# Kernel tuning notes

Hardware: AMD Instinct MI355X
Metric: run time of the kernel (lower is better)

## Reference

```python
import jax, jax.numpy as jnp
import numpy as np

CONF_THRESHOLD = 4.0
NMS_THRESHOLD = 0.5
TOP_K = 4096        # fixed candidate cap for jit-static shapes (>> expected #candidates)
NEG = -1.0e9


def setup_inputs() -> dict:
    key = jax.random.key(0)
    k1, k2, k3 = jax.random.split(key, 3)
    B, N, C = 8, 65536, 80
    logits = jax.random.normal(k1, (B, N, C), dtype=jnp.float32)
    # valid xyxy boxes in a ~1000px image: x2>x1, y2>y1
    xy = jax.random.uniform(k2, (B, N, 2), dtype=jnp.float32) * 900.0
    wh = jax.random.uniform(k3, (B, N, 2), dtype=jnp.float32) * 100.0 + 1.0
    boxes = jnp.concatenate([xy, xy + wh], axis=-1)
    return {"logits": logits, "boxes": boxes}


def _pairwise_iou(b):
    # b: [K, 4] xyxy -> [K, K] IoU (torchvision convention, no +1)
    x1, y1, x2, y2 = b[:, 0], b[:, 1], b[:, 2], b[:, 3]
    area = (x2 - x1) * (y2 - y1)                      # [K]
    iw = jnp.maximum(jnp.minimum(x2[:, None], x2[None, :]) - jnp.maximum(x1[:, None], x1[None, :]), 0.0)
    ih = jnp.maximum(jnp.minimum(y2[:, None], y2[None, :]) - jnp.maximum(y1[:, None], y1[None, :]), 0.0)
    inter = iw * ih                                   # [K, K]
    union = area[:, None] + area[None, :] - inter
    return inter / jnp.maximum(union, 1e-12)


def reference(logits, boxes):
    B, N, C = logits.shape
    scores = jnp.max(logits, axis=2)                  # [B, N]
    cls = jnp.argmax(logits, axis=2)                  # [B, N]
    # per-(image, class) NMS category id, as in the torch module
    cat = cls + jnp.arange(B, dtype=cls.dtype)[:, None] * C
    valid = scores > CONF_THRESHOLD                   # [B, N]
    img = jnp.broadcast_to(jnp.arange(B, dtype=jnp.int32)[:, None], (B, N))

    scores_f = scores.reshape(-1)
    valid_f = valid.reshape(-1)
    boxes_f = boxes.reshape(-1, 4)
    cat_f = cat.reshape(-1)
    cls_f = cls.reshape(-1)
    img_f = img.reshape(-1)

    # global descending-score order (matches batched_nms sort); invalid pushed to bottom
    vals, idx = jax.lax.top_k(jnp.where(valid_f, scores_f, NEG), TOP_K)
    bx = boxes_f[idx]                                 # [K, 4]
    ct = cat_f[idx]
    cl = cls_f[idx]
    im = img_f[idx]
    vk = valid_f[idx]                                 # [K]

    iou = _pairwise_iou(bx)                           # [K, K]
    suppress_mat = (ct[:, None] == ct[None, :]) & (iou > NMS_THRESHOLD)
    order = jnp.arange(TOP_K)

    def body(i, keep):
        sup = suppress_mat[i] & (order > i)
        return jnp.where(keep[i], keep & ~sup, keep)

    keep = jax.lax.fori_loop(0, TOP_K, body, vk)      # greedy NMS suppression

    nms_image_idx = jnp.where(keep, im, -1)
    nms_bboxes = bx * keep[:, None].astype(bx.dtype)
    nms_classes = jnp.where(keep, cl, -1)
    nms_scores = jnp.where(keep, vals, 0.0)
    return (nms_image_idx, nms_bboxes, nms_classes, nms_scores)
```

## Files before the change

kernel.cpp:

```cpp
#include <hip/hip_runtime.h>
#include <stdint.h>

typedef unsigned long long u64;
typedef unsigned int u32;
typedef float fv4 __attribute__((ext_vector_type(4)));

#define BATCH  8
#define NPTS   65536
#define NCLS   80
#define NANCH  (BATCH * NPTS)
#define TOPK   4096
#define CONF   4.0f
#define NMSTH  0.5f
#define NCAT   (BATCH * NCLS)
#define BCAP   32

static constexpr size_t OFF_CNT  = 0;
static constexpr size_t OFF_KEYS = 64;

__global__ __launch_bounds__(256, 4) void k_score(const float* __restrict__ logits,
                                                  int* __restrict__ cnt,
                                                  u64* __restrict__ keys) {
    __shared__ u32 s_sc[4][64 * 21];
    __shared__ unsigned char s_cl[4][64 * 20];
    int lane = threadIdx.x & 63;
    int w = threadIdx.x >> 6;
    int chunk = blockIdx.x * 4 + w;
    const fv4* src = (const fv4*)logits + (size_t)chunk * 1280;

    fv4 A[20];
#pragma unroll
    for (int k = 0; k < 20; ++k) A[k] = __builtin_nontemporal_load(&src[k * 64 + lane]);

    u32* sc = s_sc[w];
    unsigned char* cl = s_cl[w];

#pragma unroll
    for (int k = 0; k < 20; ++k) {
        fv4 v = A[k];
        int e = k * 64 + lane;
        float bv = v.x; int bc = 0;
        if (v.y > bv) { bv = v.y; bc = 1; }
        if (v.z > bv) { bv = v.z; bc = 2; }
        if (v.w > bv) { bv = v.w; bc = 3; }
        int a_l = e / 20, j = e % 20;
        u32 eb = __float_as_uint(bv);
        eb = (eb & 0x80000000u) ? ~eb : (eb | 0x80000000u);
        sc[a_l * 21 + j] = eb;
        cl[a_l * 20 + j] = (unsigned char)(j * 4 + bc);
    }
    u32 best = 0; int bj = 0;
#pragma unroll
    for (int j = 0; j < 20; ++j) {
        u32 p = sc[lane * 21 + j];
        if (p > best) { best = p; bj = j; }
    }
    u32 orig = (best & 0x80000000u) ? (best & 0x7fffffffu) : ~best;
    if (__uint_as_float(orig) > CONF) {
        u32 cls = cl[lane * 20 + bj];
        u32 a = (u32)chunk * 64 + (u32)lane;
        int pos = atomicAdd(cnt, 1);
        if (pos < 8192)
            keys[pos] = ((u64)best << 32) | ((((~a) & 0x7FFFFu) << 7) | cls);
    }
}

__global__ __launch_bounds__(1024) void k_nms(const int* __restrict__ cnt,
                                              const u64* __restrict__ keys_raw,
                                              const float* __restrict__ boxes,
                                              float* __restrict__ out) {
    __shared__ u64    s_keys[4096];
    __shared__ float4 s_box[4096];
    __shared__ unsigned short s_bucket[NCAT * BCAP];
    __shared__ int s_bcnt[NCAT];
    __shared__ unsigned char s_keep[4096];
    int n = min(*cnt, TOPK);
    int tid = threadIdx.x;
    int n2 = 64; while (n2 < n) n2 <<= 1;

    for (int c = tid; c < NCAT; c += 1024) s_bcnt[c] = 0;
    for (int i = tid; i < n2; i += 1024)
        s_keys[i] = (i < n) ? keys_raw[i] : 0ull;
    __syncthreads();

    for (int k = 2; k <= n2; k <<= 1) {
        for (int j = k >> 1; j > 0; j >>= 1) {
            for (int i = tid; i < n2; i += 1024) {
                int ixj = i ^ j;
                if (ixj > i) {
                    u64 x = s_keys[i], y = s_keys[ixj];
                    bool desc = ((i & k) == 0);
                    if (desc ? (x < y) : (x > y)) { s_keys[i] = y; s_keys[ixj] = x; }
                }
            }
            __syncthreads();
        }
    }

    float4 bx[4]; int cls_[4], img_[4]; float sc_[4];
#pragma unroll
    for (int r = 0; r < 4; ++r) {
        int s = tid + 1024 * r;
        float4 b = make_float4(0.f, 0.f, 0.f, 0.f);
        int cl = -1, im = -1; float v = 0.f;
        if (s < n) {
            u64 key = s_keys[s];
            u32 eb = (u32)(key >> 32);
            u32 orig = (eb & 0x80000000u) ? (eb & 0x7fffffffu) : ~eb;
            v = __uint_as_float(orig);
            u32 low = (u32)key;
            cl = (int)(low & 0x7fu);
            u32 a = (~(low >> 7)) & 0x7FFFFu;
            im = (int)(a >> 16);
            b = ((const float4*)boxes)[a];
            int c = im * NCLS + cl;
            int pos = atomicAdd(&s_bcnt[c], 1);
            if (pos < BCAP) s_bucket[c * BCAP + pos] = (unsigned short)s;
        }
        bx[r] = b; cls_[r] = cl; img_[r] = im; sc_[r] = v;
        s_box[s]  = b;
        s_keep[s] = (s < n) ? 1 : 0;
    }
    __syncthreads();

    if (tid < NCAT) {
        int m = min(s_bcnt[tid], BCAP);
        unsigned short* bkt = &s_bucket[tid * BCAP];
        if (m > 1) {
            for (int i = 1; i < m; ++i) {
                unsigned short x = bkt[i]; int j = i - 1;
                while (j >= 0 && bkt[j] > x) { bkt[j + 1] = bkt[j]; --j; }
                bkt[j + 1] = x;
            }
            for (int i = 1; i < m; ++i) {
                float4 bi = s_box[bkt[i]];
                float areai = (bi.z - bi.x) * (bi.w - bi.y);
                bool dead = false;
                for (int j = 0; j < i && !dead; ++j) {
                    if (!s_keep[bkt[j]]) continue;
                    float4 bj = s_box[bkt[j]];
                    float iw = fmaxf(fminf(bi.z, bj.z) - fmaxf(bi.x, bj.x), 0.f);
                    float ih = fmaxf(fminf(bi.w, bj.w) - fmaxf(bi.y, bj.y), 0.f);
                    float inter = iw * ih;
                    float uni = areai + (bj.z - bj.x) * (bj.w - bj.y) - inter;
                    if (inter / fmaxf(uni, 1e-12f) > NMSTH) dead = true;
                }
                if (dead) s_keep[bkt[i]] = 0;
            }
        }
    }
    __syncthreads();

#pragma unroll
    for (int r = 0; r < 4; ++r) {
        int s = tid + 1024 * r;
        bool keep = s_keep[s] != 0;
        out[s] = keep ? (float)img_[r] : -1.0f;
        ((float4*)(out + 4096))[s] = keep ? bx[r] : make_float4(0.f, 0.f, 0.f, 0.f);
        out[4096 + 16384 + s]        = keep ? (float)cls_[r] : -1.0f;
        out[4096 + 16384 + 4096 + s] = keep ? sc_[r] : 0.0f;
    }
}

extern "C" void kernel_launch(void* const* d_in, const int* in_sizes, int n_in,
                              void* d_out, int out_size, void* d_ws, size_t ws_size,
                              hipStream_t stream) {
    const float* logits = (const float*)d_in[0];
    const float* boxes  = (const float*)d_in[1];
    float* out = (float*)d_out;
    char* ws = (char*)d_ws;

    int* cnt      = (int*)(ws + OFF_CNT);
    u64* keys_raw = (u64*)(ws + OFF_KEYS);

    hipMemsetAsync(cnt, 0, 64, stream);
    k_score<<<NANCH / 256, 256, 0, stream>>>(logits, cnt, keys_raw);
    k_nms<<<1, 1024, 0, stream>>>(cnt, keys_raw, boxes, out);
}
```

Before: 270.7 us.

## Replace global atomic candidate append with per-chunk ballot slots and NMS-side compaction

The scoring kernel no longer does a global atomicAdd per candidate. Each wavefront ballots its passing anchors and writes them into a fixed 16-entry slot per 64-anchor chunk, then stores a per-chunk count. This also removes the memset. The NMS kernel reads all 8192 chunk counts and compacts the slots into shared memory with a shared atomic. This trades global atomic contention for an extra scan of the count array in the single-block NMS kernel. Candidates beyond 16 per chunk would be dropped, which is safe for the expected sparsity.

```diff
diff --git a/kernel.cpp b/kernel.cpp
--- a/kernel.cpp
+++ b/kernel.cpp
@@ -9,18 +9,20 @@
 #define NPTS   65536
 #define NCLS   80
 #define NANCH  (BATCH * NPTS)
+#define NCHUNK (NANCH / 64)
 #define TOPK   4096
 #define CONF   4.0f
 #define NMSTH  0.5f
 #define NCAT   (BATCH * NCLS)
 #define BCAP   32
-
-static constexpr size_t OFF_CNT  = 0;
-static constexpr size_t OFF_KEYS = 64;
+#define SLOT   16
+
+static constexpr size_t OFF_CNTS = 0;
+static constexpr size_t OFF_SLAB = 32768;
 
 __global__ __launch_bounds__(256, 4) void k_score(const float* __restrict__ logits,
-                                                  int* __restrict__ cnt,
-                                                  u64* __restrict__ keys) {
+                                                  u32* __restrict__ cnts,
+                                                  u64* __restrict__ slab) {
     __shared__ u32 s_sc[4][64 * 21];
     __shared__ unsigned char s_cl[4][64 * 20];
     int lane = threadIdx.x & 63;
@@ -56,17 +58,26 @@
         if (p > best) { best = p; bj = j; }
     }
     u32 orig = (best & 0x80000000u) ? (best & 0x7fffffffu) : ~best;
-    if (__uint_as_float(orig) > CONF) {
-        u32 cls = cl[lane * 20 + bj];
-        u32 a = (u32)chunk * 64 + (u32)lane;
-        int pos = atomicAdd(cnt, 1);
-        if (pos < 8192)
-            keys[pos] = ((u64)best << 32) | ((((~a) & 0x7FFFFu) << 7) | cls);
+    bool pred = __uint_as_float(orig) > CONF;
+
+    u64 ball = __ballot(pred);
+    if (pred) {
+        int slot = __popcll(ball & ((1ull << lane) - 1ull));
+        if (slot < SLOT) {
+            u32 cls = cl[lane * 20 + bj];
+            u32 a = (u32)chunk * 64 + (u32)lane;
+            slab[(size_t)chunk * SLOT + slot] =
+                ((u64)best << 32) | ((((~a) & 0x7FFFFu) << 7) | cls);
+        }
+    }
+    if (lane == 0) {
+        int m = (int)__popcll(ball);
+        cnts[chunk] = (u32)(m < SLOT ? m : SLOT);
     }
 }
 
-__global__ __launch_bounds__(1024) void k_nms(const int* __restrict__ cnt,
-                                              const u64* __restrict__ keys_raw,
+__global__ __launch_bounds__(1024) void k_nms(const u32* __restrict__ cnts,
+                                              const u64* __restrict__ slab,
                                               const float* __restrict__ boxes,
                                               float* __restrict__ out) {
     __shared__ u64    s_keys[4096];
@@ -74,14 +85,28 @@
     __shared__ unsigned short s_bucket[NCAT * BCAP];
     __shared__ int s_bcnt[NCAT];
     __shared__ unsigned char s_keep[4096];
-    int n = min(*cnt, TOPK);
+    __shared__ int s_n;
     int tid = threadIdx.x;
+
+    if (tid == 0) s_n = 0;
+    for (int c = tid; c < NCAT; c += 1024) s_bcnt[c] = 0;
+    for (int i = tid; i < 4096; i += 1024) s_keys[i] = 0ull;
+    __syncthreads();
+
+    for (int c = tid; c < NCHUNK; c += 1024) {
+        int m = (int)cnts[c];
+        if (m > 0) {
+            int pos = atomicAdd(&s_n, m);
+            for (int t = 0; t < m; ++t) {
+                int p = pos + t;
+                if (p < TOPK) s_keys[p] = slab[(size_t)c * SLOT + t];
+            }
+        }
+    }
+    __syncthreads();
+
+    int n = min(s_n, TOPK);
     int n2 = 64; while (n2 < n) n2 <<= 1;
-
-    for (int c = tid; c < NCAT; c += 1024) s_bcnt[c] = 0;
-    for (int i = tid; i < n2; i += 1024)
-        s_keys[i] = (i < n) ? keys_raw[i] : 0ull;
-    __syncthreads();
 
     for (int k = 2; k <= n2; k <<= 1) {
         for (int j = k >> 1; j > 0; j >>= 1) {
@@ -170,10 +195,9 @@
     float* out = (float*)d_out;
     char* ws = (char*)d_ws;
 
-    int* cnt      = (int*)(ws + OFF_CNT);
-    u64* keys_raw = (u64*)(ws + OFF_KEYS);
-
-    hipMemsetAsync(cnt, 0, 64, stream);
-    k_score<<<NANCH / 256, 256, 0, stream>>>(logits, cnt, keys_raw);
-    k_nms<<<1, 1024, 0, stream>>>(cnt, keys_raw, boxes, out);
+    u32* cnts = (u32*)(ws + OFF_CNTS);
+    u64* slab = (u64*)(ws + OFF_SLAB);
+
+    k_score<<<NCHUNK / 4, 256, 0, stream>>>(logits, cnts, slab);
+    k_nms<<<1, 1024, 0, stream>>>(cnts, slab, boxes, out);
 }
```

Result: no change. 274.1 us (+1.2%).
